# Kernel tuning notes

Measured on AMD Instinct MI355X. Metric: run time of the kernel, lower is better.

Reference implementation:

```python
import jax, jax.numpy as jnp
import numpy as np

B, N, F_IN, F_OUT, H = 4, 2048, 128, 256, 4
HD = F_OUT // H


def setup_inputs() -> dict:
    key = jax.random.key(0)
    k1, k2, k3, k4, k5 = jax.random.split(key, 5)
    x = jax.random.normal(k1, (B, N, F_IN), dtype=jnp.float32)
    adj = jax.random.randint(k2, (B, N, N), 0, 2, dtype=jnp.int32)
    # xavier-ish scaled params
    W = jax.random.normal(k3, (F_OUT, F_IN), dtype=jnp.float32) * float(np.sqrt(2.0 / (F_IN + F_OUT)))
    a_l = jax.random.normal(k4, (H, HD), dtype=jnp.float32) * float(np.sqrt(2.0 / (H * HD + 1)))
    a_r = jax.random.normal(k5, (H, HD), dtype=jnp.float32) * float(np.sqrt(2.0 / (H * HD + 1)))
    return {"x": x, "adj": adj, "W": W, "a_l": a_l, "a_r": a_r}


def reference(x, adj, W, a_l, a_r):
    Bb, Nn, _ = x.shape
    h = jnp.einsum('bnf,of->bno', x, W).reshape(Bb, Nn, H, HD)   # [B,N,H,HD]
    e_l = jnp.einsum('bnhd,hd->bnh', h, a_l)                      # [B,N,H]
    e_r = jnp.einsum('bnhd,hd->bnh', h, a_r)                      # [B,N,H]
    e = e_l[:, :, None, :] + e_r[:, None, :, :]                   # [B,N(i),N(j),H]
    e = jax.nn.leaky_relu(e, negative_slope=0.2)
    e = jnp.where(adj[..., None] == 0, -jnp.inf, e)
    alpha = jax.nn.softmax(e, axis=2)                             # softmax over neighbors j
    out = jnp.einsum('bijh,bjhd->bihd', alpha, h)                 # [B,N,H,HD]
    return out.reshape(Bb, Nn, F_OUT)
```

## Files before the change

### kernel.cpp

```cpp
#include <hip/hip_runtime.h>
#include <stdint.h>

#define BB 4
#define NN 2048
#define F_IN 128
#define F_OUT 256
#define NH 4
#define HD 64

typedef float f32x4 __attribute__((ext_vector_type(4)));
typedef short s16x8 __attribute__((ext_vector_type(8)));
typedef int i32x4 __attribute__((ext_vector_type(4)));
typedef unsigned long long u64;
typedef unsigned short u16;

#define LOG2E 1.4426950408889634f

__device__ __forceinline__ u16 f32_to_bf16_rtn(float f) {
    union { float f; uint32_t u; } v; v.f = f;
    uint32_t u = v.u;
    u += 0x7fffu + ((u >> 16) & 1u);
    return (u16)(u >> 16);
}

__device__ __forceinline__ float exp2_fast(float x) {
#if __has_builtin(__builtin_amdgcn_exp2f)
    return __builtin_amdgcn_exp2f(x);
#else
    return exp2f(x);
#endif
}

__device__ __forceinline__ int sbfe1(uint32_t v, int k) {
#if __has_builtin(__builtin_amdgcn_sbfe)
    return __builtin_amdgcn_sbfe((int)v, k, 1);
#else
    return ((int32_t)(v << (31 - k))) >> 31;
#endif
}

__global__ __launch_bounds__(256) void k01(
    const int* __restrict__ adj, const float* __restrict__ x,
    const float* __restrict__ W, const float* __restrict__ a_l,
    const float* __restrict__ a_r, u64* __restrict__ abits,
    u16* __restrict__ hB, float* __restrict__ el, float* __restrict__ er)
{
    const int t = threadIdx.x;

    if (blockIdx.x >= 512) {
        const int wid = ((blockIdx.x - 512) << 2) | (t >> 6);
        const int lane = t & 63;
        const int* rowp = adj + (size_t)wid * NN;
        u64 mym = 0;
#pragma unroll 8
        for (int jt = 0; jt < 32; ++jt) {
            int v = rowp[jt * 64 + lane];
            u64 m = __ballot(v != 0);
            if (lane == jt) mym = m;
        }
        if (lane < 32) abits[(size_t)wid * 32 + lane] = mym;
        return;
    }

    const int b = blockIdx.x >> 7;
    const int n0 = (blockIdx.x & 127) * 16;

    __shared__ __align__(16) float xs[16][F_IN];
    {
        const f32x4* src = (const f32x4*)(x + ((size_t)b * NN + n0) * F_IN);
        f32x4* dst = (f32x4*)&xs[0][0];
        dst[t] = src[t];
        dst[t + 256] = src[t + 256];
    }
    __syncthreads();

    float acc[16];
#pragma unroll
    for (int n = 0; n < 16; ++n) acc[n] = 0.f;

    const float* wrow = W + (size_t)t * F_IN;
#pragma unroll 2
    for (int k0 = 0; k0 < F_IN; k0 += 8) {
        f32x4 w0 = *(const f32x4*)(wrow + k0);
        f32x4 w1 = *(const f32x4*)(wrow + k0 + 4);
#pragma unroll
        for (int n = 0; n < 16; ++n) {
            f32x4 xa = *(const f32x4*)&xs[n][k0];
            f32x4 xb = *(const f32x4*)&xs[n][k0 + 4];
            float s = acc[n];
            s = fmaf(xa[0], w0[0], s); s = fmaf(xa[1], w0[1], s);
            s = fmaf(xa[2], w0[2], s); s = fmaf(xa[3], w0[3], s);
            s = fmaf(xb[0], w1[0], s); s = fmaf(xb[1], w1[1], s);
            s = fmaf(xb[2], w1[2], s); s = fmaf(xb[3], w1[3], s);
            acc[n] = s;
        }
    }

    const int w = t >> 6, lane = t & 63;
    const float al = a_l[t];
    const float ar = a_r[t];
    float my_el = 0.f, my_er = 0.f;
#pragma unroll
    for (int n = 0; n < 16; ++n) {
        float vl = acc[n] * al;
        float vr = acc[n] * ar;
#pragma unroll
        for (int off = 32; off; off >>= 1) {
            vl += __shfl_xor(vl, off, 64);
            vr += __shfl_xor(vr, off, 64);
        }
        if (lane == n) { my_el = vl; my_er = vr; }
    }
    if (lane < 16) {
        el[((size_t)b * NH + w) * NN + n0 + lane] = my_el * LOG2E;
        er[((size_t)b * NH + w) * NN + n0 + lane] = my_er * LOG2E;
    }

    const int dcol = t & 15, cb = (t >> 4) & 3;
    const int jt32 = n0 >> 5;
    const int lb = dcol + ((n0 >> 3) & 2) * 16;
    u16* hb = hB + ((((size_t)b * 64 + jt32) * 4 + w) * 4 + cb) * 512 + (size_t)lb * 8;
    s16x8 pk0, pk1;
#pragma unroll
    for (int n = 0; n < 8; ++n) pk0[n] = (short)f32_to_bf16_rtn(acc[n]);
#pragma unroll
    for (int n = 0; n < 8; ++n) pk1[n] = (short)f32_to_bf16_rtn(acc[n + 8]);
    *(s16x8*)hb         = pk0;
    *(s16x8*)(hb + 128) = pk1;
}

__global__ __launch_bounds__(256, 3) void k2_attn(
    const uint32_t* __restrict__ abits32, const u16* __restrict__ hB,
    const float* __restrict__ el, const float* __restrict__ er,
    float* __restrict__ out)
{
    const int t = threadIdx.x;
    const int jq = t >> 6, l = t & 63;
    int bid = blockIdx.x;
    bid = (bid & 7) * 128 + (bid >> 3);
    const int b = bid >> 8;
    const int w = (bid >> 6) & 3;
    const int i0 = (bid & 63) * 32;
    const int r = l & 15;
    const int kb = l >> 4;
    const int ks = kb * 8;
    const int irow0 = i0 + r, irow1 = irow0 + 16;

    const u16* hbp = hB + ((((size_t)b * 64 + jq * 16) * 4 + w) * 4) * 512 + (size_t)l * 8;
    const float* errp = er + ((size_t)b * NH + w) * NN + jq * 512 + ks;
    const i32x4* m0p4 = (const i32x4*)(abits32 + ((size_t)b * NN + irow0) * 64 + jq * 16);
    const i32x4* m1p4 = (const i32x4*)(abits32 + ((size_t)b * NN + irow1) * 64 + jq * 16);

    const float el_i0 = el[((size_t)b * NH + w) * NN + irow0];
    const float el_i1 = el[((size_t)b * NH + w) * NN + irow1];

    f32x4 a00 = {0.f,0.f,0.f,0.f}, a01 = a00, a02 = a00, a03 = a00, as0 = a00;
    f32x4 a10 = a00, a11 = a00, a12 = a00, a13 = a00, as1 = a00;
    s16x8 ones;
#pragma unroll
    for (int k = 0; k < 8; ++k) ones[k] = (short)0x3F80;

    i32x4 mg0c = m0p4[0], mg1c = m1p4[0];
    s16x8 b0c = *(const s16x8*)(hbp + 0 * 512);
    s16x8 b1c = *(const s16x8*)(hbp + 1 * 512);
    s16x8 b2c = *(const s16x8*)(hbp + 2 * 512);
    s16x8 b3c = *(const s16x8*)(hbp + 3 * 512);
    __builtin_amdgcn_sched_barrier(0);

#define MFMA_BF16 __builtin_amdgcn_mfma_f32_16x16x32_bf16
#define BODY(IT, S, PF)                                                       \
    {                                                                         \
                                               \
        const float* ep_ = errp + (IT) * 32;                                  \
        f32x4 e0_ = *(const f32x4*)ep_;                                       \
        f32x4 e1_ = *(const f32x4*)(ep_ + 4);                                 \
        s16x8 b0n, b1n, b2n, b3n;                                             \
        if (PF) {                                      \
            const u16* hp_ = hbp + (size_t)((IT) + 1) * 8192;                 \
            b0n = *(const s16x8*)(hp_ + 0 * 512);                             \
            b1n = *(const s16x8*)(hp_ + 1 * 512);                             \
            b2n = *(const s16x8*)(hp_ + 2 * 512);                             \
            b3n = *(const s16x8*)(hp_ + 3 * 512);                             \
        }                                                                     \
        __builtin_amdgcn_sched_barrier(0);                                    \
        uint32_t w2a = ((uint32_t)mg0c[S]) >> ks;                             \
        uint32_t w2b = ((uint32_t)mg1c[S]) >> ks;                             \
        uint32_t pua[8], pub[8];                                              \
        _Pragma("unroll")                                                     \
        for (int k = 0; k < 8; ++k) {                                         \
            float e_j = (k < 4) ? e0_[k] : e1_[k - 4];                        \
            float s0 = el_i0 + e_j;                                           \
            float s1 = el_i1 + e_j;                                           \
            s0 = fmaxf(s0, 0.2f * s0);                                        \
            s1 = fmaxf(s1, 0.2f * s1);                                        \
            float p0 = exp2_fast(s0);                                         \
            float p1 = exp2_fast(s1);                                         \
            union { float f; uint32_t u; } c0, c1; c0.f = p0; c1.f = p1;      \
            pua[k] = c0.u & (uint32_t)sbfe1(w2a, k);                          \
            pub[k] = c1.u & (uint32_t)sbfe1(w2b, k);                          \
        }                                                                     \
        union { s16x8 v; uint32_t u[4]; } afa, afb;                           \
        afa.u[0] = __builtin_amdgcn_perm(pua[1], pua[0], 0x07060302);         \
        afa.u[1] = __builtin_amdgcn_perm(pua[3], pua[2], 0x07060302);         \
        afa.u[2] = __builtin_amdgcn_perm(pua[5], pua[4], 0x07060302);         \
        afa.u[3] = __builtin_amdgcn_perm(pua[7], pua[6], 0x07060302);         \
        afb.u[0] = __builtin_amdgcn_perm(pub[1], pub[0], 0x07060302);         \
        afb.u[1] = __builtin_amdgcn_perm(pub[3], pub[2], 0x07060302);         \
        afb.u[2] = __builtin_amdgcn_perm(pub[5], pub[4], 0x07060302);         \
        afb.u[3] = __builtin_amdgcn_perm(pub[7], pub[6], 0x07060302);         \
        a00 = MFMA_BF16(afa.v, b0c, a00, 0, 0, 0);                            \
        a01 = MFMA_BF16(afa.v, b1c, a01, 0, 0, 0);                            \
        a02 = MFMA_BF16(afa.v, b2c, a02, 0, 0, 0);                            \
        a03 = MFMA_BF16(afa.v, b3c, a03, 0, 0, 0);                            \
        as0 = MFMA_BF16(afa.v, ones, as0, 0, 0, 0);                           \
        a10 = MFMA_BF16(afb.v, b0c, a10, 0, 0, 0);                            \
        a11 = MFMA_BF16(afb.v, b1c, a11, 0, 0, 0);                            \
        a12 = MFMA_BF16(afb.v, b2c, a12, 0, 0, 0);                            \
        a13 = MFMA_BF16(afb.v, b3c, a13, 0, 0, 0);                            \
        as1 = MFMA_BF16(afb.v, ones, as1, 0, 0, 0);                           \
        if (PF) { b0c = b0n; b1c = b1n; b2c = b2n; b3c = b3n; }               \
    }

    for (int g = 0; g < 3; ++g) {
        i32x4 mg0n = m0p4[g + 1];
        i32x4 mg1n = m1p4[g + 1];
        __builtin_amdgcn_sched_barrier(0);
#pragma unroll
        for (int s = 0; s < 4; ++s) {
            const int it = g * 4 + s;
            BODY(it, s, 1);
        }
        mg0c = mg0n; mg1c = mg1n;
    }
#pragma unroll
    for (int s = 0; s < 4; ++s) {
        const int it = 12 + s;
        if (s < 3) { BODY(it, s, 1); } else { BODY(it, s, 0); }
    }

    __shared__ __align__(16) float racc[3 * 64 * 44];
    if (jq > 0) {
        float* p = &racc[((jq - 1) * 64 + l) * 44];
        *(f32x4*)(p +  0) = a00; *(f32x4*)(p +  4) = a01;
        *(f32x4*)(p +  8) = a02; *(f32x4*)(p + 12) = a03;
        *(f32x4*)(p + 16) = as0;
        *(f32x4*)(p + 20) = a10; *(f32x4*)(p + 24) = a11;
        *(f32x4*)(p + 28) = a12; *(f32x4*)(p + 32) = a13;
        *(f32x4*)(p + 36) = as1;
    }
    __syncthreads();
    if (jq == 0) {
#pragma unroll
        for (int s = 0; s < 3; ++s) {
            const float* p = &racc[(s * 64 + l) * 44];
            a00 += *(const f32x4*)(p +  0); a01 += *(const f32x4*)(p +  4);
            a02 += *(const f32x4*)(p +  8); a03 += *(const f32x4*)(p + 12);
            as0 += *(const f32x4*)(p + 16);
            a10 += *(const f32x4*)(p + 20); a11 += *(const f32x4*)(p + 24);
            a12 += *(const f32x4*)(p + 28); a13 += *(const f32x4*)(p + 32);
            as1 += *(const f32x4*)(p + 36);
        }

        float* op = out + ((size_t)b * NN + i0) * F_OUT + w * HD;
#pragma unroll
        for (int q = 0; q < 4; ++q) {
            const int row0 = kb * 4 + q;
            float inv0 = 1.0f / as0[q];
            op[(size_t)row0 * F_OUT +  0 + r] = a00[q] * inv0;
            op[(size_t)row0 * F_OUT + 16 + r] = a01[q] * inv0;
            op[(size_t)row0 * F_OUT + 32 + r] = a02[q] * inv0;
            op[(size_t)row0 * F_OUT + 48 + r] = a03[q] * inv0;
            const int row1 = 16 + kb * 4 + q;
            float inv1 = 1.0f / as1[q];
            op[(size_t)row1 * F_OUT +  0 + r] = a10[q] * inv1;
            op[(size_t)row1 * F_OUT + 16 + r] = a11[q] * inv1;
            op[(size_t)row1 * F_OUT + 32 + r] = a12[q] * inv1;
            op[(size_t)row1 * F_OUT + 48 + r] = a13[q] * inv1;
        }
    }
}

extern "C" void kernel_launch(void* const* d_in, const int* in_sizes, int n_in,
                              void* d_out, int out_size, void* d_ws, size_t ws_size,
                              hipStream_t stream) {
    const float* x   = (const float*)d_in[0];
    const int*   adj = (const int*)d_in[1];
    const float* W   = (const float*)d_in[2];
    const float* a_l = (const float*)d_in[3];
    const float* a_r = (const float*)d_in[4];
    float* out = (float*)d_out;

    char* ws = (char*)d_ws;
    u16*   hB    = (u16*)ws;
    u64*   abits = (u64*)(ws + (size_t)BB * F_OUT * NN * 2);
    float* el    = (float*)(ws + (size_t)BB * F_OUT * NN * 2 + (size_t)BB * NN * 32 * 8);
    float* er    = el + (size_t)BB * NH * NN;

    k01<<<512 + BB * NN / 4, 256, 0, stream>>>(adj, x, W, a_l, a_r, abits, hB, el, er);
    k2_attn<<<BB * NH * (NN / 32), 256, 0, stream>>>((const uint32_t*)abits, hB, el, er, out);
}
```

Before: 50.68 us.

## Prefetch er values one iteration ahead and reduce el/er via LDS

In the attention kernel, the er vector loads move into the software-prefetch stage so they are issued one iteration ahead, together with the hB loads. This hides their latency behind the exp and MFMA work instead of stalling at the start of each body. In the projection kernel, the per-node 64-lane shuffle reductions for el/er are replaced by a transposed partial-sum pass through shared memory plus two shuffles. The cost is extra LDS (about 40KB more per block, also allocated for the bitmask-packing blocks), a block-wide barrier, and more registers for the prefetched vectors.

Result: faster. 46.87 us (-7.5%).

```diff
diff --git a/kernel.cpp b/kernel.cpp
--- a/kernel.cpp
+++ b/kernel.cpp
@@ -46,6 +46,10 @@
     u16* __restrict__ hB, float* __restrict__ el, float* __restrict__ er)
 {
     const int t = threadIdx.x;
+
+    __shared__ __align__(16) float xs[16][F_IN];
+    __shared__ __align__(16) float redl[4 * 64 * 20];
+    __shared__ __align__(16) float redr[4 * 64 * 20];
 
     if (blockIdx.x >= 512) {
         const int wid = ((blockIdx.x - 512) << 2) | (t >> 6);
@@ -65,7 +69,6 @@
     const int b = blockIdx.x >> 7;
     const int n0 = (blockIdx.x & 127) * 16;
 
-    __shared__ __align__(16) float xs[16][F_IN];
     {
         const f32x4* src = (const f32x4*)(x + ((size_t)b * NN + n0) * F_IN);
         f32x4* dst = (f32x4*)&xs[0][0];
@@ -99,21 +102,37 @@
     const int w = t >> 6, lane = t & 63;
     const float al = a_l[t];
     const float ar = a_r[t];
-    float my_el = 0.f, my_er = 0.f;
-#pragma unroll
-    for (int n = 0; n < 16; ++n) {
-        float vl = acc[n] * al;
-        float vr = acc[n] * ar;
-#pragma unroll
-        for (int off = 32; off; off >>= 1) {
-            vl += __shfl_xor(vl, off, 64);
-            vr += __shfl_xor(vr, off, 64);
-        }
-        if (lane == n) { my_el = vl; my_er = vr; }
-    }
-    if (lane < 16) {
-        el[((size_t)b * NH + w) * NN + n0 + lane] = my_el * LOG2E;
-        er[((size_t)b * NH + w) * NN + n0 + lane] = my_er * LOG2E;
+    {
+        float* rl = &redl[((size_t)w * 64 + lane) * 20];
+        float* rr = &redr[((size_t)w * 64 + lane) * 20];
+#pragma unroll
+        for (int q = 0; q < 4; ++q) {
+            f32x4 vl, vr;
+#pragma unroll
+            for (int e = 0; e < 4; ++e) {
+                vl[e] = acc[q * 4 + e] * al;
+                vr[e] = acc[q * 4 + e] * ar;
+            }
+            *(f32x4*)(rl + q * 4) = vl;
+            *(f32x4*)(rr + q * 4) = vr;
+        }
+    }
+    __syncthreads();
+    {
+        const int n_ = lane & 15, og = lane >> 4;
+        float sl = 0.f, sr = 0.f;
+#pragma unroll
+        for (int oo = 0; oo < 16; ++oo) {
+            const int o = og + 4 * oo;
+            sl += redl[((size_t)w * 64 + o) * 20 + n_];
+            sr += redr[((size_t)w * 64 + o) * 20 + n_];
+        }
+        sl += __shfl_xor(sl, 16, 64); sl += __shfl_xor(sl, 32, 64);
+        sr += __shfl_xor(sr, 16, 64); sr += __shfl_xor(sr, 32, 64);
+        if (lane < 16) {
+            el[((size_t)b * NH + w) * NN + n0 + lane] = sl * LOG2E;
+            er[((size_t)b * NH + w) * NN + n0 + lane] = sr * LOG2E;
+        }
     }
 
     const int dcol = t & 15, cb = (t >> 4) & 3;
@@ -165,22 +184,24 @@
     s16x8 b1c = *(const s16x8*)(hbp + 1 * 512);
     s16x8 b2c = *(const s16x8*)(hbp + 2 * 512);
     s16x8 b3c = *(const s16x8*)(hbp + 3 * 512);
+    f32x4 e0c = *(const f32x4*)errp;
+    f32x4 e1c = *(const f32x4*)(errp + 4);
     __builtin_amdgcn_sched_barrier(0);
 
 #define MFMA_BF16 __builtin_amdgcn_mfma_f32_16x16x32_bf16
 #define BODY(IT, S, PF)                                                       \
     {                                                                         \
-                                               \
-        const float* ep_ = errp + (IT) * 32;                                  \
-        f32x4 e0_ = *(const f32x4*)ep_;                                       \
-        f32x4 e1_ = *(const f32x4*)(ep_ + 4);                                 \
         s16x8 b0n, b1n, b2n, b3n;                                             \
-        if (PF) {                                      \
+        f32x4 e0n, e1n;                                                       \
+        if (PF) {                         \
             const u16* hp_ = hbp + (size_t)((IT) + 1) * 8192;                 \
             b0n = *(const s16x8*)(hp_ + 0 * 512);                             \
             b1n = *(const s16x8*)(hp_ + 1 * 512);                             \
             b2n = *(const s16x8*)(hp_ + 2 * 512);                             \
             b3n = *(const s16x8*)(hp_ + 3 * 512);                             \
+            const float* ep_ = errp + ((IT) + 1) * 32;                        \
+            e0n = *(const f32x4*)ep_;                                         \
+            e1n = *(const f32x4*)(ep_ + 4);                                   \
         }                                                                     \
         __builtin_amdgcn_sched_barrier(0);                                    \
         uint32_t w2a = ((uint32_t)mg0c[S]) >> ks;                             \
@@ -188,7 +209,7 @@
         uint32_t pua[8], pub[8];                                              \
         _Pragma("unroll")                                                     \
         for (int k = 0; k < 8; ++k) {                                         \
-            float e_j = (k < 4) ? e0_[k] : e1_[k - 4];                        \
+            float e_j = (k < 4) ? e0c[k] : e1c[k - 4];                        \
             float s0 = el_i0 + e_j;                                           \
             float s1 = el_i1 + e_j;                                           \
             s0 = fmaxf(s0, 0.2f * s0);                                        \
@@ -218,7 +239,8 @@
         a12 = MFMA_BF16(afb.v, b2c, a12, 0, 0, 0);                            \
         a13 = MFMA_BF16(afb.v, b3c, a13, 0, 0, 0);                            \
         as1 = MFMA_BF16(afb.v, ones, as1, 0, 0, 0);                           \
-        if (PF) { b0c = b0n; b1c = b1n; b2c = b2n; b3c = b3n; }               \
+        if (PF) { b0c = b0n; b1c = b1n; b2c = b2n; b3c = b3n;                 \
+                  e0c = e0n; e1c = e1n; }                                     \
     }
 
     for (int g = 0; g < 3; ++g) {
```
